# Kernel tuning notes

Measured on AMD Instinct MI355X. Metric: run time of the kernel, lower is better.

Reference implementation:

```python
import jax, jax.numpy as jnp
import numpy as np

TEMPERATURE = 0.07
ALPHA = 0.5
TOP_K = 5
SIGMA = 2.0
SCALES = (1, 2, 4)
CL_WEIGHT = 1.0
EPS = 1e-9
NORM_EPS = 1e-12  # F.normalize default eps


def _multi_scale_diffusion(z, scales=SCALES):
    """Row-stochastic affinity from cosine similarity, averaged matrix powers.
    z: [B,N,D] -> assoc: [B,N,N]. (multi_scale_diffusion was external in the
    original repo; this is the standard formulation.)"""
    zn = z / (jnp.linalg.norm(z, axis=-1, keepdims=True) + NORM_EPS)
    sim = jnp.einsum('bnd,bmd->bnm', zn, zn)          # [B,N,N]
    A = jax.nn.softmax(sim, axis=-1)                   # row-stochastic transition
    acc = jnp.zeros_like(A)
    cur, p = A, 1
    for s in sorted(scales):                           # static, tiny loop
        while p < s:
            cur = jnp.einsum('bnk,bkm->bnm', cur, A)   # A^p
            p += 1
        acc = acc + cur
    return acc / float(len(scales))


def _distance_weight(N, sigma):
    idx = jnp.arange(N, dtype=jnp.float32)
    d = idx[:, None] - idx[None, :]
    return jnp.exp(-(d * d) / (2.0 * sigma * sigma))   # [N,N]


def _half_numerator(scores, cross, strong, ar):
    # scores: [B,N,N] extension scores; cross: exp_sim block [B,N,N];
    # strong: [B,N] strong-positive exp_sim; ar: arange(N)
    vals, idx = jax.lax.top_k(scores, TOP_K)           # [B,N,K]
    gath = jnp.take_along_axis(cross, idx, axis=-1)    # [B,N,K]
    mask = (idx != ar[None, :, None]).astype(scores.dtype)  # skip strong positive
    return strong + (mask * vals * gath).sum(-1)       # [B,N]


def reference(proj_z1, proj_z2):
    B, N, D = proj_z1.shape
    assoc1 = _multi_scale_diffusion(proj_z1)
    assoc2 = _multi_scale_diffusion(proj_z2)
    pw = _distance_weight(N, SIGMA)                    # [N,N]

    z_cat = jnp.concatenate([proj_z1, proj_z2], axis=1)        # [B,2N,D]
    z_cat = z_cat / (jnp.linalg.norm(z_cat, axis=-1, keepdims=True) + NORM_EPS)
    sim = jnp.einsum('bnd,bmd->bnm', z_cat, z_cat)             # [B,2N,2N]
    exp_sim = jnp.exp(sim / TEMPERATURE)

    den = exp_sim.sum(-1) - jnp.diagonal(exp_sim, axis1=1, axis2=2)  # [B,2N]
    ar = jnp.arange(N)

    # rows i < N: positives live in view2 (columns N:2N), extension via assoc2
    scores1 = ALPHA * pw[None] + (1.0 - ALPHA) * assoc2        # [B,N,N]
    cross12 = exp_sim[:, :N, N:]                               # [B,N,N]
    strong1 = jnp.diagonal(cross12, axis1=1, axis2=2)          # exp_sim[i, i+N]
    num1 = _half_numerator(scores1, cross12, strong1, ar)

    # rows i >= N: positives live in view1 (columns 0:N), extension via assoc1
    scores2 = ALPHA * pw[None] + (1.0 - ALPHA) * assoc1
    cross21 = exp_sim[:, N:, :N]
    strong2 = jnp.diagonal(cross21, axis1=1, axis2=2)          # exp_sim[i+N, i]
    num2 = _half_numerator(scores2, cross21, strong2, ar)

    num = jnp.concatenate([num1, num2], axis=1)                # [B,2N]
    loss = -jnp.log(num / (den + EPS) + EPS)
    return CL_WEIGHT * loss.mean()


def setup_inputs() -> dict:
    key = jax.random.key(0)
    k1, k2 = jax.random.split(key)
    B, N, D = 16, 1024, 256
    return {
        'proj_z1': jax.random.normal(k1, (B, N, D), dtype=jnp.float32),
        'proj_z2': jax.random.normal(k2, (B, N, D), dtype=jnp.float32),
    }
```

## Files before the change

kernel.cpp:

```cpp
#include <hip/hip_runtime.h>
#include <cmath>
#include <cstdint>

#define BB 16
#define NN_ 1024
#define DD 256

constexpr float INV_T = 1.0f / 0.07f;

typedef __attribute__((ext_vector_type(8))) short bf16x8;
typedef __attribute__((ext_vector_type(4))) float f32x4;

static __device__ __forceinline__ float b2f(ushort u) {
  union { uint i; float f; } c; c.i = ((uint)u) << 16; return c.f;
}
static __device__ __forceinline__ ushort f2b(float f) {
  union { float f; uint i; } c; c.f = f;
  uint r = c.i + 0x7fffu + ((c.i >> 16) & 1u);
  return (ushort)(r >> 16);
}

static __device__ __forceinline__ void gload16(const void* g, void* l) {
  __builtin_amdgcn_global_load_lds((const __attribute__((address_space(1))) unsigned int*)g,
                                   (__attribute__((address_space(3))) unsigned int*)l, 16, 0, 0);
}

__global__ __launch_bounds__(256) void k_norm(const float* __restrict__ z1, const float* __restrict__ z2,
                                              ushort* __restrict__ znAll) {
  const int row = blockIdx.x;
  const int t = threadIdx.x;
  const bool second = row >= BB * NN_;
  const float* z = second ? z2 : z1;
  const size_t inBase = (size_t)(second ? row - BB * NN_ : row) * DD + t;
  float v = z[inBase];
  float ss = v * v;
#pragma unroll
  for (int o = 32; o; o >>= 1) ss += __shfl_xor(ss, o);
  __shared__ float par[4];
  if ((t & 63) == 0) par[t >> 6] = ss;
  __syncthreads();
  float tot = par[0] + par[1] + par[2] + par[3];
  znAll[(size_t)row * DD + t] = f2b(v / (sqrtf(tot) + 1e-12f));
}

template <int MODE, int K, int TRI>
__global__ __launch_bounds__(256) void k_gemm_nt(const ushort* __restrict__ U, const ushort* __restrict__ V,
                                                 ushort* __restrict__ C, float* __restrict__ denR,
                                                 float* __restrict__ denC, float* __restrict__ rsum) {
  __shared__ __align__(16) ushort smem[17408];
  ushort (*As)[128][32] = (ushort (*)[128][32])smem;
  ushort (*Bs)[128][32] = (ushort (*)[128][32])(smem + 8192);
  ushort (*tb)[136] = (ushort (*)[136])smem;

  const int t = threadIdx.x;
  const int fid = blockIdx.x;
  const int xcd = fid & 7;
  int b, row0, col0;
  if constexpr (TRI) {
    int j = fid >> 3;
    const int half = (j >= 36) ? 1 : 0;
    b = (xcd << 1) | half;
    int rem = j - half * 36;
    int r = 0;
#pragma unroll
    for (int q = 0; q < 7; ++q) {
      if (rem >= 8 - r) { rem -= 8 - r; ++r; }
    }
    row0 = r << 7;
    col0 = (r + rem) << 7;
  } else {
    const int j = fid >> 3;
    b = (xcd << 1) | (j >> 6);
    const int jj = j & 63;
    row0 = (jj >> 3) << 7;
    col0 = (jj & 7) << 7;
  }

  const size_t ub = (size_t)b * NN_ * K;
  const size_t cb = (size_t)b * NN_ * NN_;
  const int lane = t & 63, w = t >> 6;
  const int wr = w >> 1, wc = w & 1;
  const int l15 = lane & 15, slot = lane >> 4;

  const int sRow = lane >> 2;
  const int kg = (lane & 3) ^ ((lane >> 3) & 3);
  const int sCol = kg << 3;
  const ushort* gA0 = U + ub + (size_t)(row0 + (w << 5) + sRow) * K + sCol;
  const ushort* gA1 = gA0 + (size_t)16 * K;
  const ushort* gB0 = V + ub + (size_t)(col0 + (w << 5) + sRow) * K + sCol;
  const ushort* gB1 = gB0 + (size_t)16 * K;

  f32x4 acc[4][4];
#pragma unroll
  for (int i = 0; i < 4; ++i)
#pragma unroll
    for (int jx = 0; jx < 4; ++jx)
#pragma unroll
      for (int e = 0; e < 4; ++e) acc[i][jx][e] = 0.f;

  gload16(gA0, &As[0][w << 5][0]);
  gload16(gA1, &As[0][(w << 5) + 16][0]);
  gload16(gB0, &Bs[0][w << 5][0]);
  gload16(gB1, &Bs[0][(w << 5) + 16][0]);
  __syncthreads();

  int cur = 0;
  for (int k0 = 0; k0 < K; k0 += 32) {
    const int nxt = cur ^ 1;
    if (k0 + 32 < K) {
      gload16(gA0 + k0 + 32, &As[nxt][w << 5][0]);
      gload16(gA1 + k0 + 32, &As[nxt][(w << 5) + 16][0]);
      gload16(gB0 + k0 + 32, &Bs[nxt][w << 5][0]);
      gload16(gB1 + k0 + 32, &Bs[nxt][(w << 5) + 16][0]);
    }
    bf16x8 af[4], bfv[4];
#pragma unroll
    for (int fr = 0; fr < 4; ++fr) {
      const int r = (wr << 6) + (fr << 4) + l15;
      af[fr] = *(const bf16x8*)&As[cur][r][(slot ^ ((r >> 1) & 3)) << 3];
    }
#pragma unroll
    for (int fc = 0; fc < 4; ++fc) {
      const int r = (wc << 6) + (fc << 4) + l15;
      bfv[fc] = *(const bf16x8*)&Bs[cur][r][(slot ^ ((r >> 1) & 3)) << 3];
    }
#pragma unroll
    for (int fr = 0; fr < 4; ++fr)
#pragma unroll
      for (int fc = 0; fc < 4; ++fc)
        acc[fr][fc] = __builtin_amdgcn_mfma_f32_16x16x32_bf16(af[fr], bfv[fc], acc[fr][fc], 0, 0, 0);
    __syncthreads();
    cur = nxt;
  }

  if constexpr (MODE == 2) {
    float colp[4] = {0.f, 0.f, 0.f, 0.f};
#pragma unroll
    for (int fr = 0; fr < 4; ++fr) {
#pragma unroll
      for (int jx = 0; jx < 4; ++jx) {
        const int grow = row0 + (wr << 6) + (fr << 4) + (slot << 2) + jx;
        float rs = 0.f;
#pragma unroll
        for (int fc = 0; fc < 4; ++fc) {
          const float e = expf(acc[fr][fc][jx] * INV_T);
          rs += e;
          colp[fc] += e;
        }
#pragma unroll
        for (int o = 1; o < 16; o <<= 1) rs += __shfl_xor(rs, o);
        if (l15 == 0) atomicAdd(&denR[(size_t)b * NN_ + grow], rs);
      }
    }
#pragma unroll
    for (int fc = 0; fc < 4; ++fc) {
      float cs = colp[fc];
      cs += __shfl_xor(cs, 16);
      cs += __shfl_xor(cs, 32);
      if (slot == 0) atomicAdd(&denC[(size_t)b * NN_ + col0 + (wc << 6) + (fc << 4) + l15], cs);
    }
  } else if constexpr (MODE == 1) {
    float colp_d[4] = {0.f, 0.f, 0.f, 0.f};
    float colp_e[4] = {0.f, 0.f, 0.f, 0.f};
#pragma unroll
    for (int fr = 0; fr < 4; ++fr) {
#pragma unroll
      for (int jx = 0; jx < 4; ++jx) {
        const int lrow = (wr << 6) + (fr << 4) + (slot << 2) + jx;
        const int grow = row0 + lrow;
        float rs = 0.f, es = 0.f;
#pragma unroll
        for (int fc = 0; fc < 4; ++fc) {
          const int lcol = (wc << 6) + (fc << 4) + l15;
          const int gcol = col0 + lcol;
          const float v = acc[fr][fc][jx];
          const float ev = expf(v);
          const ushort h = f2b(ev);
          C[cb + (size_t)grow * NN_ + gcol] = h;
          tb[lcol][lrow] = h;
          es += ev;
          colp_e[fc] += ev;
          const float dv = expf(v * INV_T);
          if (grow != gcol) { rs += dv; colp_d[fc] += dv; }
        }
#pragma unroll
        for (int o = 1; o < 16; o <<= 1) { rs += __shfl_xor(rs, o); es += __shfl_xor(es, o); }
        if (l15 == 0) {
          atomicAdd(&denR[(size_t)b * NN_ + grow], rs);
          atomicAdd(&rsum[(size_t)b * NN_ + grow], es);
        }
      }
    }
    if (row0 != col0) {
#pragma unroll
      for (int fc = 0; fc < 4; ++fc) {
        float cd = colp_d[fc], ce = colp_e[fc];
        cd += __shfl_xor(cd, 16); cd += __shfl_xor(cd, 32);
        ce += __shfl_xor(ce, 16); ce += __shfl_xor(ce, 32);
        if (slot == 0) {
          const int gcol = col0 + (wc << 6) + (fc << 4) + l15;
          atomicAdd(&denR[(size_t)b * NN_ + gcol], cd);
          atomicAdd(&rsum[(size_t)b * NN_ + gcol], ce);
        }
      }
      __syncthreads();
#pragma unroll
      for (int rep = 0; rep < 8; ++rep) {
        const int cid = rep * 256 + t;
        const int rr = cid >> 4;
        const int c8 = (cid & 15) << 3;
        *(uint4*)&C[cb + (size_t)(col0 + rr) * NN_ + row0 + c8] = *(const uint4*)&tb[rr][c8];
      }
    }
  } else {
#pragma unroll
    for (int fr = 0; fr < 4; ++fr) {
#pragma unroll
      for (int jx = 0; jx < 4; ++jx) {
        const int lrow = (wr << 6) + (fr << 4) + (slot << 2) + jx;
        const int grow = row0 + lrow;
#pragma unroll
        for (int fc = 0; fc < 4; ++fc) {
          const int lcol = (wc << 6) + (fc << 4) + l15;
          const ushort h = f2b(acc[fr][fc][jx]);
          C[cb + (size_t)grow * NN_ + col0 + lcol] = h;
          if constexpr (TRI) tb[lcol][lrow] = h;
        }
      }
    }
    if constexpr (TRI) {
      if (row0 != col0) {
        __syncthreads();
#pragma unroll
        for (int rep = 0; rep < 8; ++rep) {
          const int cid = rep * 256 + t;
          const int rr = cid >> 4;
          const int c8 = (cid & 15) << 3;
          *(uint4*)&C[cb + (size_t)(col0 + rr) * NN_ + row0 + c8] = *(const uint4*)&tb[rr][c8];
        }
      }
    }
  }
}

__global__ __launch_bounds__(256) void k_scale(ushort* __restrict__ E, const float* __restrict__ r) {
  const size_t idx8 = ((size_t)blockIdx.x * 256 + threadIdx.x) << 3;
  const int grow = (int)(idx8 >> 10);
  const int bcol = (int)(idx8 & 1023);
  const int batch = grow >> 10;
  const float rsi = rsqrtf(r[grow]);
  bf16x8 v = *(const bf16x8*)&E[idx8];
  const float* rb = r + (batch << 10) + bcol;
  const float4 rc0 = *(const float4*)rb;
  const float4 rc1 = *(const float4*)(rb + 4);
  float rj[8] = {rc0.x, rc0.y, rc0.z, rc0.w, rc1.x, rc1.y, rc1.z, rc1.w};
  bf16x8 o;
#pragma unroll
  for (int e = 0; e < 8; ++e) {
    const float wgt = rsi * rsqrtf(rj[e]);
    o[e] = (short)f2b(b2f((ushort)v[e]) * wgt);
  }
  *(bf16x8*)&E[idx8] = o;
}

__global__ __launch_bounds__(256) void k_loss(const ushort* __restrict__ M, const ushort* __restrict__ M2,
                                              const float* __restrict__ r, const ushort* __restrict__ znS,
                                              const ushort* __restrict__ znO, const float* __restrict__ den,
                                              float* __restrict__ lossRows, int halfOff) {
  const int row = (blockIdx.x << 2) + (threadIdx.x >> 6);
  const int lane = threadIdx.x & 63;
  const int b = row >> 10, i = row & 1023;
  const size_t mb = (size_t)b * NN_ * NN_;
  const int w0 = min(max(i - 2, 0), NN_ - 5);

  const ushort* zr = M2 + mb + (size_t)i * NN_ + (lane << 4);
  const bf16x8 r0 = *(const bf16x8*)zr;
  const bf16x8 r1 = *(const bf16x8*)(zr + 8);

  const ushort4 qv = *(const ushort4*)&znS[((size_t)b * NN_ + i) * DD + (lane << 2)];
  const float q0 = b2f(qv.x), q1 = b2f(qv.y), q2 = b2f(qv.z), q3 = b2f(qv.w);

  float a4[5], cd[5];
#pragma unroll
  for (int s = 0; s < 5; ++s) {
    const int j = w0 + s;
    float p = 0.f;
    if (j != i) {
      const ushort* wrp = M2 + mb + (size_t)j * NN_ + (lane << 4);
      const bf16x8 wv0 = *(const bf16x8*)wrp;
      const bf16x8 wv1 = *(const bf16x8*)(wrp + 8);
#pragma unroll
      for (int e = 0; e < 8; ++e)
        p += b2f((ushort)r0[e]) * b2f((ushort)wv0[e]) + b2f((ushort)r1[e]) * b2f((ushort)wv1[e]);
    }
    const ushort4 ov = *(const ushort4*)&znO[((size_t)b * NN_ + j) * DD + (lane << 2)];
    float c = q0 * b2f(ov.x) + q1 * b2f(ov.y) + q2 * b2f(ov.z) + q3 * b2f(ov.w);
#pragma unroll
    for (int o = 32; o; o >>= 1) { p += __shfl_xor(p, o); c += __shfl_xor(c, o); }
    a4[s] = p;
    cd[s] = c;
  }

  const float rsi = rsqrtf(r[(size_t)b * NN_ + i]);
  float num = 0.f;
#pragma unroll
  for (int s = 0; s < 5; ++s) {
    const int j = w0 + s;
    const float g = expf(cd[s] * INV_T);
    if (j == i) {
      num += g;
    } else {
      const float d = (float)(j - i);
      const float pw = expf(-d * d * 0.125f);
      const float ratio = sqrtf(r[(size_t)b * NN_ + j]) * rsi;
      const float mband = b2f(M[mb + (size_t)i * NN_ + j]);
      const float m2band = b2f(M2[mb + (size_t)i * NN_ + j]);
      const float sc = 0.5f * pw + ratio * (mband + m2band + a4[s]) * (0.5f / 3.0f);
      num += sc * g;
    }
  }

  if (lane == 0) {
    const float dn = den[(size_t)b * NN_ + i];
    lossRows[(size_t)b * (2 * NN_) + halfOff + i] = -logf(num / (dn + 1e-9f) + 1e-9f);
  }
}

__global__ __launch_bounds__(256) void k_final(const float* __restrict__ lossRows, float* __restrict__ out) {
  const int t = threadIdx.x;
  float s = 0.f;
  for (int idx = t; idx < BB * 2 * NN_; idx += 256) s += lossRows[idx];
#pragma unroll
  for (int o = 32; o; o >>= 1) s += __shfl_xor(s, o);
  __shared__ float p[4];
  if ((t & 63) == 0) p[t >> 6] = s;
  __syncthreads();
  if (t == 0) out[0] = (p[0] + p[1] + p[2] + p[3]) / (float)(BB * 2 * NN_);
}

extern "C" void kernel_launch(void* const* d_in, const int* in_sizes, int n_in, void* d_out, int out_size,
                              void* d_ws, size_t ws_size, hipStream_t stream) {
  const float* z1 = (const float*)d_in[0];
  const float* z2 = (const float*)d_in[1];
  float* out = (float*)d_out;

  const size_t nzd = (size_t)BB * NN_ * DD;
  const size_t nnn = (size_t)BB * NN_ * NN_;
  const size_t nv = (size_t)BB * NN_;

  ushort* zn1 = (ushort*)d_ws;
  ushort* zn2 = zn1 + nzd;
  ushort* X = zn2 + nzd;
  ushort* Y = X + nnn;
  ushort* Z = Y + nnn;
  float* den1 = (float*)(Z + nnn);
  float* den2 = den1 + nv;
  float* rsum1 = den2 + nv;
  float* rsum2 = rsum1 + nv;
  float* lossRows = rsum2 + nv;

  const size_t needed = 2 * nzd * 2 + 3 * nnn * 2 + 6 * nv * 4;
  if (ws_size < needed) return;

  dim3 blk(256);
  const int gTri = 36 * 2 * 8;
  const int gFull = 64 * 2 * 8;
  const int gScale = (int)(nnn / 2048);
  const int gLoss = (int)(nv / 4);

  hipMemsetAsync(den1, 0, 4 * nv * 4, stream);

  k_norm<<<2 * BB * NN_, blk, 0, stream>>>(z1, z2, zn1);

  k_gemm_nt<1, DD, 1><<<gTri, blk, 0, stream>>>(zn2, zn2, X, den2, nullptr, rsum2);
  k_scale<<<gScale, blk, 0, stream>>>(X, rsum2);
  k_gemm_nt<0, NN_, 1><<<gTri, blk, 0, stream>>>(X, X, Z, nullptr, nullptr, nullptr);

  k_gemm_nt<2, DD, 0><<<gFull, blk, 0, stream>>>(zn1, zn2, nullptr, den1, den2, nullptr);

  k_gemm_nt<1, DD, 1><<<gTri, blk, 0, stream>>>(zn1, zn1, Y, den1, nullptr, rsum1);
  k_scale<<<gScale, blk, 0, stream>>>(Y, rsum1);

  k_loss<<<gLoss, blk, 0, stream>>>(X, Z, rsum2, zn1, zn2, den1, lossRows, 0);

  k_gemm_nt<0, NN_, 1><<<gTri, blk, 0, stream>>>(Y, Y, Z, nullptr, nullptr, nullptr);

  k_loss<<<gLoss, blk, 0, stream>>>(Y, Z, rsum1, zn2, zn1, den2, lossRows, NN_);

  k_final<<<1, blk, 0, stream>>>(lossRows, out);
}
```

Before: 326.5 us.

## Batch both views into merged GEMM, scale, square and loss launches

Merges the two per-view self-similarity GEMMs and the cross-view GEMM into one launch, and does the same for the scale, squared-affinity GEMM and loss kernels, so each stage covers both views in a single grid. The memset is folded into the norm kernel, and the loss rows are written over the den buffers. The aim is to cut the launch count and fill the GPU better, since each old per-view grid was small (576 blocks). The cost is a second Z buffer in the workspace (more memory) and runtime branching inside the combined kernel.

```diff
diff --git a/kernel.cpp b/kernel.cpp
--- a/kernel.cpp
+++ b/kernel.cpp
@@ -26,9 +26,10 @@
 }
 
 __global__ __launch_bounds__(256) void k_norm(const float* __restrict__ z1, const float* __restrict__ z2,
-                                              ushort* __restrict__ znAll) {
+                                              ushort* __restrict__ znAll, float* __restrict__ vecs) {
   const int row = blockIdx.x;
   const int t = threadIdx.x;
+  if (row < 256) vecs[(row << 8) + t] = 0.f;
   const bool second = row >= BB * NN_;
   const float* z = second ? z2 : z1;
   const size_t inBase = (size_t)(second ? row - BB * NN_ : row) * DD + t;
@@ -43,10 +44,9 @@
   znAll[(size_t)row * DD + t] = f2b(v / (sqrtf(tot) + 1e-12f));
 }
 
-template <int MODE, int K, int TRI>
-__global__ __launch_bounds__(256) void k_gemm_nt(const ushort* __restrict__ U, const ushort* __restrict__ V,
-                                                 ushort* __restrict__ C, float* __restrict__ denR,
-                                                 float* __restrict__ denC, float* __restrict__ rsum) {
+__global__ __launch_bounds__(256) void k_mega256(const ushort* __restrict__ znAll, ushort* __restrict__ XY,
+                                                 float* __restrict__ den1, float* __restrict__ den2,
+                                                 float* __restrict__ rsum1, float* __restrict__ rsum2) {
   __shared__ __align__(16) ushort smem[17408];
   ushort (*As)[128][32] = (ushort (*)[128][32])smem;
   ushort (*Bs)[128][32] = (ushort (*)[128][32])(smem + 8192);
@@ -54,41 +54,54 @@
 
   const int t = threadIdx.x;
   const int fid = blockIdx.x;
-  const int xcd = fid & 7;
-  int b, row0, col0;
-  if constexpr (TRI) {
-    int j = fid >> 3;
-    const int half = (j >= 36) ? 1 : 0;
-    b = (xcd << 1) | half;
-    int rem = j - half * 36;
+  const bool isSim = fid < 1152;
+  const size_t nzd = (size_t)BB * NN_ * DD;
+  int b, row0, col0, m = 0;
+  const ushort *baseA, *baseB;
+  ushort* C = nullptr;
+  float *denR, *denC = nullptr, *rsum = nullptr;
+  if (isSim) {
+    const int xcd = fid & 7;
+    const int j = fid >> 3;
+    const int unit = j / 36;
+    int rem = j % 36;
+    m = unit >> 1;
+    b = (xcd << 1) | (unit & 1);
     int r = 0;
 #pragma unroll
-    for (int q = 0; q < 7; ++q) {
+    for (int q = 0; q < 7; ++q)
       if (rem >= 8 - r) { rem -= 8 - r; ++r; }
-    }
     row0 = r << 7;
     col0 = (r + rem) << 7;
+    baseA = znAll + (m ? 0 : nzd) + (size_t)b * NN_ * DD;
+    baseB = baseA;
+    C = XY + (size_t)m * BB * NN_ * NN_ + (size_t)b * NN_ * NN_;
+    denR = m ? den1 : den2;
+    rsum = m ? rsum1 : rsum2;
   } else {
-    const int j = fid >> 3;
+    const int f2 = fid - 1152;
+    const int xcd = f2 & 7;
+    const int j = f2 >> 3;
     b = (xcd << 1) | (j >> 6);
     const int jj = j & 63;
     row0 = (jj >> 3) << 7;
     col0 = (jj & 7) << 7;
-  }
-
-  const size_t ub = (size_t)b * NN_ * K;
-  const size_t cb = (size_t)b * NN_ * NN_;
+    baseA = znAll + (size_t)b * NN_ * DD;
+    baseB = znAll + nzd + (size_t)b * NN_ * DD;
+    denR = den1;
+    denC = den2;
+  }
+
   const int lane = t & 63, w = t >> 6;
   const int wr = w >> 1, wc = w & 1;
   const int l15 = lane & 15, slot = lane >> 4;
-
   const int sRow = lane >> 2;
   const int kg = (lane & 3) ^ ((lane >> 3) & 3);
   const int sCol = kg << 3;
-  const ushort* gA0 = U + ub + (size_t)(row0 + (w << 5) + sRow) * K + sCol;
-  const ushort* gA1 = gA0 + (size_t)16 * K;
-  const ushort* gB0 = V + ub + (size_t)(col0 + (w << 5) + sRow) * K + sCol;
-  const ushort* gB1 = gB0 + (size_t)16 * K;
+  const ushort* gA0 = baseA + (size_t)(row0 + (w << 5) + sRow) * DD + sCol;
+  const ushort* gA1 = gA0 + (size_t)16 * DD;
+  const ushort* gB0 = baseB + (size_t)(col0 + (w << 5) + sRow) * DD + sCol;
+  const ushort* gB1 = gB0 + (size_t)16 * DD;
 
   f32x4 acc[4][4];
 #pragma unroll
@@ -105,9 +118,9 @@
   __syncthreads();
 
   int cur = 0;
-  for (int k0 = 0; k0 < K; k0 += 32) {
+  for (int k0 = 0; k0 < DD; k0 += 32) {
     const int nxt = cur ^ 1;
-    if (k0 + 32 < K) {
+    if (k0 + 32 < DD) {
       gload16(gA0 + k0 + 32, &As[nxt][w << 5][0]);
       gload16(gA1 + k0 + 32, &As[nxt][(w << 5) + 16][0]);
       gload16(gB0 + k0 + 32, &Bs[nxt][w << 5][0]);
@@ -133,33 +146,7 @@
     cur = nxt;
   }
 
-  if constexpr (MODE == 2) {
-    float colp[4] = {0.f, 0.f, 0.f, 0.f};
-#pragma unroll
-    for (int fr = 0; fr < 4; ++fr) {
-#pragma unroll
-      for (int jx = 0; jx < 4; ++jx) {
-        const int grow = row0 + (wr << 6) + (fr << 4) + (slot << 2) + jx;
-        float rs = 0.f;
-#pragma unroll
-        for (int fc = 0; fc < 4; ++fc) {
-          const float e = expf(acc[fr][fc][jx] * INV_T);
-          rs += e;
-          colp[fc] += e;
-        }
-#pragma unroll
-        for (int o = 1; o < 16; o <<= 1) rs += __shfl_xor(rs, o);
-        if (l15 == 0) atomicAdd(&denR[(size_t)b * NN_ + grow], rs);
-      }
-    }
-#pragma unroll
-    for (int fc = 0; fc < 4; ++fc) {
-      float cs = colp[fc];
-      cs += __shfl_xor(cs, 16);
-      cs += __shfl_xor(cs, 32);
-      if (slot == 0) atomicAdd(&denC[(size_t)b * NN_ + col0 + (wc << 6) + (fc << 4) + l15], cs);
-    }
-  } else if constexpr (MODE == 1) {
+  if (isSim) {
     float colp_d[4] = {0.f, 0.f, 0.f, 0.f};
     float colp_e[4] = {0.f, 0.f, 0.f, 0.f};
 #pragma unroll
@@ -176,7 +163,7 @@
           const float v = acc[fr][fc][jx];
           const float ev = expf(v);
           const ushort h = f2b(ev);
-          C[cb + (size_t)grow * NN_ + gcol] = h;
+          C[(size_t)grow * NN_ + gcol] = h;
           tb[lcol][lrow] = h;
           es += ev;
           colp_e[fc] += ev;
@@ -209,47 +196,50 @@
         const int cid = rep * 256 + t;
         const int rr = cid >> 4;
         const int c8 = (cid & 15) << 3;
-        *(uint4*)&C[cb + (size_t)(col0 + rr) * NN_ + row0 + c8] = *(const uint4*)&tb[rr][c8];
+        *(uint4*)&C[(size_t)(col0 + rr) * NN_ + row0 + c8] = *(const uint4*)&tb[rr][c8];
       }
     }
   } else {
+    float colp[4] = {0.f, 0.f, 0.f, 0.f};
 #pragma unroll
     for (int fr = 0; fr < 4; ++fr) {
 #pragma unroll
       for (int jx = 0; jx < 4; ++jx) {
-        const int lrow = (wr << 6) + (fr << 4) + (slot << 2) + jx;
-        const int grow = row0 + lrow;
+        const int grow = row0 + (wr << 6) + (fr << 4) + (slot << 2) + jx;
+        float rs = 0.f;
 #pragma unroll
         for (int fc = 0; fc < 4; ++fc) {
-          const int lcol = (wc << 6) + (fc << 4) + l15;
-          const ushort h = f2b(acc[fr][fc][jx]);
-          C[cb + (size_t)grow * NN_ + col0 + lcol] = h;
-          if constexpr (TRI) tb[lcol][lrow] = h;
+          const float e = expf(acc[fr][fc][jx] * INV_T);
+          rs += e;
+          colp[fc] += e;
         }
+#pragma unroll
+        for (int o = 1; o < 16; o <<= 1) rs += __shfl_xor(rs, o);
+        if (l15 == 0) atomicAdd(&denR[(size_t)b * NN_ + grow], rs);
       }
     }
-    if constexpr (TRI) {
-      if (row0 != col0) {
-        __syncthreads();
-#pragma unroll
-        for (int rep = 0; rep < 8; ++rep) {
-          const int cid = rep * 256 + t;
-          const int rr = cid >> 4;
-          const int c8 = (cid & 15) << 3;
-          *(uint4*)&C[cb + (size_t)(col0 + rr) * NN_ + row0 + c8] = *(const uint4*)&tb[rr][c8];
-        }
-      }
-    }
-  }
-}
-
-__global__ __launch_bounds__(256) void k_scale(ushort* __restrict__ E, const float* __restrict__ r) {
+#pragma unroll
+    for (int fc = 0; fc < 4; ++fc) {
+      float cs = colp[fc];
+      cs += __shfl_xor(cs, 16);
+      cs += __shfl_xor(cs, 32);
+      if (slot == 0) atomicAdd(&denC[(size_t)b * NN_ + col0 + (wc << 6) + (fc << 4) + l15], cs);
+    }
+  }
+}
+
+__global__ __launch_bounds__(256) void k_scale(ushort* __restrict__ XY, const float* __restrict__ rsum1,
+                                               const float* __restrict__ rsum2) {
   const size_t idx8 = ((size_t)blockIdx.x * 256 + threadIdx.x) << 3;
-  const int grow = (int)(idx8 >> 10);
-  const int bcol = (int)(idx8 & 1023);
+  const size_t nnn = (size_t)BB * NN_ * NN_;
+  const int m = idx8 >= nnn;
+  const float* r = m ? rsum1 : rsum2;
+  const size_t loc = idx8 - (size_t)m * nnn;
+  const int grow = (int)(loc >> 10);
+  const int bcol = (int)(loc & 1023);
   const int batch = grow >> 10;
   const float rsi = rsqrtf(r[grow]);
-  bf16x8 v = *(const bf16x8*)&E[idx8];
+  bf16x8 v = *(const bf16x8*)&XY[idx8];
   const float* rb = r + (batch << 10) + bcol;
   const float4 rc0 = *(const float4*)rb;
   const float4 rc1 = *(const float4*)(rb + 4);
@@ -260,20 +250,135 @@
     const float wgt = rsi * rsqrtf(rj[e]);
     o[e] = (short)f2b(b2f((ushort)v[e]) * wgt);
   }
-  *(bf16x8*)&E[idx8] = o;
-}
-
-__global__ __launch_bounds__(256) void k_loss(const ushort* __restrict__ M, const ushort* __restrict__ M2,
-                                              const float* __restrict__ r, const ushort* __restrict__ znS,
-                                              const ushort* __restrict__ znO, const float* __restrict__ den,
-                                              float* __restrict__ lossRows, int halfOff) {
-  const int row = (blockIdx.x << 2) + (threadIdx.x >> 6);
+  *(bf16x8*)&XY[idx8] = o;
+}
+
+__global__ __launch_bounds__(256) void k_megasq(const ushort* __restrict__ XY, ushort* __restrict__ ZW) {
+  __shared__ __align__(16) ushort smem[17408];
+  ushort (*As)[128][32] = (ushort (*)[128][32])smem;
+  ushort (*Bs)[128][32] = (ushort (*)[128][32])(smem + 8192);
+  ushort (*tb)[136] = (ushort (*)[136])smem;
+
+  const int t = threadIdx.x;
+  const int fid = blockIdx.x;
+  const int xcd = fid & 7;
+  const int j = fid >> 3;
+  const int unit = j / 36;
+  int rem = j % 36;
+  const int m = unit >> 1;
+  const int b = (xcd << 1) | (unit & 1);
+  int r = 0;
+#pragma unroll
+  for (int q = 0; q < 7; ++q)
+    if (rem >= 8 - r) { rem -= 8 - r; ++r; }
+  const int row0 = r << 7;
+  const int col0 = (r + rem) << 7;
+
+  const size_t nnn = (size_t)BB * NN_ * NN_;
+  const ushort* baseA = XY + (size_t)m * nnn + (size_t)b * NN_ * NN_;
+  ushort* C = ZW + (size_t)m * nnn + (size_t)b * NN_ * NN_;
+
+  const int lane = t & 63, w = t >> 6;
+  const int wr = w >> 1, wc = w & 1;
+  const int l15 = lane & 15, slot = lane >> 4;
+  const int sRow = lane >> 2;
+  const int kg = (lane & 3) ^ ((lane >> 3) & 3);
+  const int sCol = kg << 3;
+  const ushort* gA0 = baseA + (size_t)(row0 + (w << 5) + sRow) * NN_ + sCol;
+  const ushort* gA1 = gA0 + (size_t)16 * NN_;
+  const ushort* gB0 = baseA + (size_t)(col0 + (w << 5) + sRow) * NN_ + sCol;
+  const ushort* gB1 = gB0 + (size_t)16 * NN_;
+
+  f32x4 acc[4][4];
+#pragma unroll
+  for (int i = 0; i < 4; ++i)
+#pragma unroll
+    for (int jx = 0; jx < 4; ++jx)
+#pragma unroll
+      for (int e = 0; e < 4; ++e) acc[i][jx][e] = 0.f;
+
+  gload16(gA0, &As[0][w << 5][0]);
+  gload16(gA1, &As[0][(w << 5) + 16][0]);
+  gload16(gB0, &Bs[0][w << 5][0]);
+  gload16(gB1, &Bs[0][(w << 5) + 16][0]);
+  __syncthreads();
+
+  int cur = 0;
+  for (int k0 = 0; k0 < NN_; k0 += 32) {
+    const int nxt = cur ^ 1;
+    if (k0 + 32 < NN_) {
+      gload16(gA0 + k0 + 32, &As[nxt][w << 5][0]);
+      gload16(gA1 + k0 + 32, &As[nxt][(w << 5) + 16][0]);
+      gload16(gB0 + k0 + 32, &Bs[nxt][w << 5][0]);
+      gload16(gB1 + k0 + 32, &Bs[nxt][(w << 5) + 16][0]);
+    }
+    bf16x8 af[4], bfv[4];
+#pragma unroll
+    for (int fr = 0; fr < 4; ++fr) {
+      const int rr = (wr << 6) + (fr << 4) + l15;
+      af[fr] = *(const bf16x8*)&As[cur][rr][(slot ^ ((rr >> 1) & 3)) << 3];
+    }
+#pragma unroll
+    for (int fc = 0; fc < 4; ++fc) {
+      const int rr = (wc << 6) + (fc << 4) + l15;
+      bfv[fc] = *(const bf16x8*)&Bs[cur][rr][(slot ^ ((rr >> 1) & 3)) << 3];
+    }
+#pragma unroll
+    for (int fr = 0; fr < 4; ++fr)
+#pragma unroll
+      for (int fc = 0; fc < 4; ++fc)
+        acc[fr][fc] = __builtin_amdgcn_mfma_f32_16x16x32_bf16(af[fr], bfv[fc], acc[fr][fc], 0, 0, 0);
+    __syncthreads();
+    cur = nxt;
+  }
+
+#pragma unroll
+  for (int fr = 0; fr < 4; ++fr) {
+#pragma unroll
+    for (int jx = 0; jx < 4; ++jx) {
+      const int lrow = (wr << 6) + (fr << 4) + (slot << 2) + jx;
+      const int grow = row0 + lrow;
+#pragma unroll
+      for (int fc = 0; fc < 4; ++fc) {
+        const int lcol = (wc << 6) + (fc << 4) + l15;
+        const ushort h = f2b(acc[fr][fc][jx]);
+        C[(size_t)grow * NN_ + col0 + lcol] = h;
+        tb[lcol][lrow] = h;
+      }
+    }
+  }
+  if (row0 != col0) {
+    __syncthreads();
+#pragma unroll
+    for (int rep = 0; rep < 8; ++rep) {
+      const int cid = rep * 256 + t;
+      const int rr = cid >> 4;
+      const int c8 = (cid & 15) << 3;
+      *(uint4*)&C[(size_t)(col0 + rr) * NN_ + row0 + c8] = *(const uint4*)&tb[rr][c8];
+    }
+  }
+}
+
+__global__ __launch_bounds__(256) void k_megaloss(const ushort* __restrict__ XY, const ushort* __restrict__ ZW,
+                                                  const ushort* __restrict__ znAll,
+                                                  const float* __restrict__ rsum1, const float* __restrict__ rsum2,
+                                                  float* __restrict__ den1, float* __restrict__ den2) {
+  const int gid = (blockIdx.x << 2) + (threadIdx.x >> 6);
   const int lane = threadIdx.x & 63;
-  const int b = row >> 10, i = row & 1023;
-  const size_t mb = (size_t)b * NN_ * NN_;
+  const int h = gid >> 14;
+  const int lr = gid & 16383;
+  const int b = lr >> 10, i = lr & 1023;
+  const size_t nnn = (size_t)BB * NN_ * NN_;
+  const size_t nzd = (size_t)BB * NN_ * DD;
+  const ushort* M = XY + (size_t)h * nnn + (size_t)b * NN_ * NN_;
+  const ushort* M2 = ZW + (size_t)h * nnn + (size_t)b * NN_ * NN_;
+  const float* r = h ? rsum1 : rsum2;
+  float* den = h ? den2 : den1;
+  const ushort* znS = znAll + (size_t)h * nzd;
+  const ushort* znO = znAll + (size_t)(1 - h) * nzd;
   const int w0 = min(max(i - 2, 0), NN_ - 5);
 
-  const ushort* zr = M2 + mb + (size_t)i * NN_ + (lane << 4);
+  const ushort* zr = M2 + (size_t)i * NN_ + (lane << 4);
   const bf16x8 r0 = *(const bf16x8*)zr;
   const bf16x8 r1 = *(const bf16x8*)(zr + 8);
 
@@ -283,17 +388,17 @@
   float a4[5], cd[5];
 #pragma unroll
   for (int s = 0; s < 5; ++s) {
-    const int j = w0 + s;
+    const int jx = w0 + s;
     float p = 0.f;
-    if (j != i) {
-      const ushort* wrp = M2 + mb + (size_t)j * NN_ + (lane << 4);
+    if (jx != i) {
+      const ushort* wrp = M2 + (size_t)jx * NN_ + (lane << 4);
       const bf16x8 wv0 = *(const bf16x8*)wrp;
       const bf16x8 wv1 = *(const bf16x8*)(wrp + 8);
 #pragma unroll
       for (int e = 0; e < 8; ++e)
         p += b2f((ushort)r0[e]) * b2f((ushort)wv0[e]) + b2f((ushort)r1[e]) * b2f((ushort)wv1[e]);
     }
-    const ushort4 ov = *(const ushort4*)&znO[((size_t)b * NN_ + j) * DD + (lane << 2)];
+    const ushort4 ov = *(const ushort4*)&znO[((size_t)b * NN_ + jx) * DD + (lane << 2)];
     float c = q0 * b2f(ov.x) + q1 * b2f(ov.y) + q2 * b2f(ov.z) + q3 * b2f(ov.w);
 #pragma unroll
     for (int o = 32; o; o >>= 1) { p += __shfl_xor(p, o); c += __shfl_xor(c, o); }
@@ -305,16 +410,16 @@
   float num = 0.f;
 #pragma unroll
   for (int s = 0; s < 5; ++s) {
-    const int j = w0 + s;
+    const int jx = w0 + s;
     const float g = expf(cd[s] * INV_T);
-    if (j == i) {
+    if (jx == i) {
       num += g;
     } else {
-      const float d = (float)(j - i);
+      const float d = (float)(jx - i);
       const float pw = expf(-d * d * 0.125f);
-      const float ratio = sqrtf(r[(size_t)b * NN_ + j]) * rsi;
-      const float mband = b2f(M[mb + (size_t)i * NN_ + j]);
-      const float m2band = b2f(M2[mb + (size_t)i * NN_ + j]);
+      const float ratio = sqrtf(r[(size_t)b * NN_ + jx]) * rsi;
+      const float mband = b2f(M[(size_t)i * NN_ + jx]);
+      const float m2band = b2f(M2[(size_t)i * NN_ + jx]);
       const float sc = 0.5f * pw + ratio * (mband + m2band + a4[s]) * (0.5f / 3.0f);
       num += sc * g;
     }
@@ -322,7 +427,7 @@
 
   if (lane == 0) {
     const float dn = den[(size_t)b * NN_ + i];
-    lossRows[(size_t)b * (2 * NN_) + halfOff + i] = -logf(num / (dn + 1e-9f) + 1e-9f);
+    den[(size_t)b * NN_ + i] = -logf(num / (dn + 1e-9f) + 1e-9f);
   }
 }
 
@@ -348,44 +453,28 @@
   const size_t nnn = (size_t)BB * NN_ * NN_;
   const size_t nv = (size_t)BB * NN_;
 
-  ushort* zn1 = (ushort*)d_ws;
-  ushort* zn2 = zn1 + nzd;
-  ushort* X = zn2 + nzd;
-  ushort* Y = X + nnn;
-  ushort* Z = Y + nnn;
-  float* den1 = (float*)(Z + nnn);
+  ushort* znAll = (ushort*)d_ws;
+  ushort* XY = znAll + 2 * nzd;
+  ushort* ZW = XY + 2 * nnn;
+  float* den1 = (float*)(ZW + 2 * nnn);
   float* den2 = den1 + nv;
   float* rsum1 = den2 + nv;
   float* rsum2 = rsum1 + nv;
-  float* lossRows = rsum2 + nv;
-
-  const size_t needed = 2 * nzd * 2 + 3 * nnn * 2 + 6 * nv * 4;
+
+  const size_t needed = 2 * nzd * 2 + 4 * nnn * 2 + 4 * nv * 4;
   if (ws_size < needed) return;
 
   dim3 blk(256);
-  const int gTri = 36 * 2 * 8;
-  const int gFull = 64 * 2 * 8;
-  const int gScale = (int)(nnn / 2048);
-  const int gLoss = (int)(nv / 4);
-
-  hipMemsetAsync(den1, 0, 4 * nv * 4, stream);
-
-  k_norm<<<2 * BB * NN_, blk, 0, stream>>>(z1, z2, zn1);
-
-  k_gemm_nt<1, DD, 1><<<gTri, blk, 0, stream>>>(zn2, zn2, X, den2, nullptr, rsum2);
-  k_scale<<<gScale, blk, 0, stream>>>(X, rsum2);
-  k_gemm_nt<0, NN_, 1><<<gTri, blk, 0, stream>>>(X, X, Z, nullptr, nullptr, nullptr);
-
-  k_gemm_nt<2, DD, 0><<<gFull, blk, 0, stream>>>(zn1, zn2, nullptr, den1, den2, nullptr);
-
-  k_gemm_nt<1, DD, 1><<<gTri, blk, 0, stream>>>(zn1, zn1, Y, den1, nullptr, rsum1);
-  k_scale<<<gScale, blk, 0, stream>>>(Y, rsum1);
-
-  k_loss<<<gLoss, blk, 0, stream>>>(X, Z, rsum2, zn1, zn2, den1, lossRows, 0);
-
-  k_gemm_nt<0, NN_, 1><<<gTri, blk, 0, stream>>>(Y, Y, Z, nullptr, nullptr, nullptr);
-
-  k_loss<<<gLoss, blk, 0, stream>>>(Y, Z, rsum1, zn2, zn1, den2, lossRows, NN_);
-
-  k_final<<<1, blk, 0, stream>>>(lossRows, out);
-}
+
+  k_norm<<<2 * BB * NN_, blk, 0, stream>>>(z1, z2, znAll, den1);
+
+  k_mega256<<<1152 + 1024, blk, 0, stream>>>(znAll, XY, den1, den2, rsum1, rsum2);
+
+  k_scale<<<(int)(2 * nnn / 2048), blk, 0, stream>>>(XY, rsum1, rsum2);
+
+  k_megasq<<<1152, blk, 0, stream>>>(XY, ZW);
+
+  k_megaloss<<<(int)(2 * nv / 4), blk, 0, stream>>>(XY, ZW, znAll, rsum1, rsum2, den1, den2);
+
+  k_final<<<1, blk, 0, stream>>>(den1, out);
+}
```

New measurement: 296.4 us. 9.2% less time.
